# Optimization experiments

Hardware: AMD Instinct MI355X
Metric: run time of the kernel (lower is better)

The kernel has to match this reference:

```python
import jax, jax.numpy as jnp
import numpy as np

B, C_IN, N_IN, N_OUT = 4, 64, 8192, 8192
D1, F, H = 4, 15, 16384  # d+1, filter_size, max_hash_cnt
C_MID, C_OUT = 64, 64
LEAK = 0.01


def setup_inputs() -> dict:
    key = jax.random.key(0)
    ks = jax.random.split(key, 10)
    features = jax.random.normal(ks[0], (B, C_IN, N_IN), jnp.float32)
    in_barycentric = jax.random.uniform(ks[1], (B, D1, N_IN), dtype=jnp.float32)
    # global flat lattice offsets: local vertex id in [0,H) plus per-batch base b*(H+1)
    local_off = jax.random.randint(ks[2], (B, D1, N_IN), 0, H)
    base = (jnp.arange(B, dtype=jnp.int64) * (H + 1))[:, None, None]
    in_lattice_offset = local_off.astype(jnp.int64) + base
    # neighbor ids in [-1, H); -1 means missing -> maps to zero padding slot after +1
    blur_neighbors = (jax.random.randint(ks[3], (B, F, H), 0, H + 1) - 1).astype(jnp.int64)
    out_barycentric = jax.random.uniform(ks[4], (B, D1, N_OUT), dtype=jnp.float32)
    out_lattice_offset = jax.random.randint(ks[5], (B, D1, N_OUT), 0, H).astype(jnp.int64)
    # blur conv params: layer0 Conv2d(C_IN,C_MID,(F,1)) + LeakyReLU, layer1 Conv2d(C_MID,C_OUT,(1,1)) no relu
    W0 = jax.random.normal(ks[6], (C_MID, C_IN, F), jnp.float32) * 0.05
    b0 = jax.random.normal(ks[7], (C_MID,), jnp.float32) * 0.01
    W1 = jax.random.normal(ks[8], (C_OUT, C_MID), jnp.float32) * 0.1
    b1 = jax.random.normal(ks[9], (C_OUT,), jnp.float32) * 0.01
    bias = jnp.zeros((C_OUT,), jnp.float32)  # slice bias, initialized to zeros as in module
    return dict(features=features, in_barycentric=in_barycentric,
                in_lattice_offset=in_lattice_offset, blur_neighbors=blur_neighbors,
                out_barycentric=out_barycentric, out_lattice_offset=out_lattice_offset,
                W0=W0, b0=b0, W1=W1, b1=b1, bias=bias)


def reference(features, in_barycentric, in_lattice_offset, blur_neighbors,
              out_barycentric, out_lattice_offset, W0, b0, W1, b1, bias):
    b_sz, c_in, n_in = features.shape
    max_hash = blur_neighbors.shape[-1]
    # ---- splat: scatter-sum barycentric-weighted features onto lattice vertices ----
    vals = in_barycentric[:, None, :, :] * features[:, :, None, :]      # (B,C,d1,N)
    vals = vals.transpose(0, 2, 3, 1).reshape(-1, c_in)                  # (B*d1*N, C)
    idx = (in_lattice_offset + 1).reshape(-1)                            # (B*d1*N,)
    splat = jax.ops.segment_sum(vals, idx, num_segments=b_sz * (max_hash + 1))
    splat = splat.reshape(b_sz, max_hash + 1, c_in).transpose(0, 2, 1)   # (B,C,H+1)
    # normalization: splat of all-ones feature
    one_splat = jax.ops.segment_sum(in_barycentric.reshape(-1), idx,
                                    num_segments=b_sz * (max_hash + 1))
    one_splat = one_splat.reshape(b_sz, max_hash + 1)
    splat = splat / (one_splat + 1e-5)[:, None, :]
    # ---- blur: gather F neighbors per vertex, then conv over the filter axis ----
    spread = jax.vmap(lambda s, n: s[:, n])(splat, blur_neighbors + 1)   # (B,C,F,H)
    h0 = jnp.einsum('bcfh,ocf->boh', spread, W0) + b0[None, :, None]     # (B,C_mid,H)
    h0 = jnp.where(h0 > 0, h0, LEAK * h0)                                # LeakyReLU
    feat_blurred = jnp.einsum('boh,po->bph', h0, W1) + b1[None, :, None] # (B,C_out,H)
    # ---- slice: barycentric-weighted gather back to output points ----
    tmp = jax.vmap(lambda f, o: f[:, o])(feat_blurred, out_lattice_offset)  # (B,C_out,d1,N_out)
    sliced = (out_barycentric[:, None, :, :] * tmp).sum(axis=2)
    sliced = sliced + bias[None, :, None]
    return sliced
```

## Files before the change

kernel.cpp:

```cpp
#include <hip/hip_runtime.h>

#define NB 4
#define C_IN 64
#define N_IN 8192
#define N_OUT 8192
#define D1 4
#define FS 15
#define HSZ 16384
#define C_MID 64
#define C_OUT 64
#define LEAK 0.01f
#define CAP 24

#define NVERT (NB*(HSZ+1))

typedef __attribute__((ext_vector_type(8))) short short8;
typedef __attribute__((ext_vector_type(4))) float floatx4;

#define SPLATB_OFF 0
#define SPLATB_FL  (NVERT*32)
#define W0B_OFF    (SPLATB_OFF + SPLATB_FL)
#define W0B_FL     (C_MID*C_IN*FS/2)
#define W1B_OFF    (W0B_OFF + W0B_FL)
#define W1B_FL     (C_OUT*C_MID/2)
#define BREG_OFF   (W1B_OFF + W1B_FL)
#define FEATB_OFF  (BREG_OFF)
#define FEATB_FL   (NB*N_IN*32)
#define CNT_OFF    (FEATB_OFF + FEATB_FL)
#define CNT_FL     (NVERT)
#define ENTID_OFF  (CNT_OFF + CNT_FL)
#define ENT_FL     (NVERT*CAP)
#define ENTW_OFF   (ENTID_OFF + ENT_FL)
#define FB_OFF     (BREG_OFF)
#define FB_FL      (NB*HSZ*32)

__device__ inline ushort f2bf(float x) {
    uint u = __float_as_uint(x);
    return (ushort)((u + 0x7FFF + ((u >> 16) & 1)) >> 16);
}
__device__ inline float bf2f(ushort b) {
    return __uint_as_float(((uint)b) << 16);
}

__global__ __launch_bounds__(256) void prep(const float* __restrict__ feat,
                                            const float* __restrict__ W0,
                                            const float* __restrict__ W1,
                                            const int* __restrict__ off,
                                            const float* __restrict__ bary,
                                            ushort* __restrict__ featB,
                                            ushort* __restrict__ W0b,
                                            ushort* __restrict__ W1b,
                                            int* __restrict__ cnt,
                                            int* __restrict__ ent_id,
                                            float* __restrict__ ent_w) {
    __shared__ float t[64 * 65];
    const int blk = blockIdx.x;
    const int tid = threadIdx.x;
    if (blk < 512) {
        const int b  = blk >> 7;
        const int nb = (blk & 127) << 6;
        const int l  = tid & 63;
        const int g  = tid >> 6;
#pragma unroll
        for (int i = 0; i < 16; ++i) {
            int c = g * 16 + i;
            t[c * 65 + l] = feat[((size_t)(b * 64 + c)) * N_IN + nb + l];
        }
        __syncthreads();
#pragma unroll
        for (int i = 0; i < 16; ++i) {
            int n = g * 16 + i;
            featB[((size_t)(b * N_IN) + nb + n) * 64 + l] = f2bf(t[l * 65 + n]);
        }
    } else if (blk < 1024) {
        int e = (blk - 512) * 256 + tid;
        int v = off[e] + 1;
        int n = e % N_IN;
        int b = e / (D1 * N_IN);
        int slot = atomicAdd(&cnt[v], 1);
        if (slot < CAP) {
            ent_id[v * CAP + slot] = b * N_IN + n;
            ent_w [v * CAP + slot] = bary[e];
        }
    } else {
        int e = (blk - 1024) * 256 + tid;
        if (e < C_MID * C_IN * FS) {
            int f = e >> 12;
            int o = (e >> 6) & 63;
            int c = e & 63;
            W0b[e] = f2bf(W0[(o * 64 + c) * FS + f]);
        } else {
            int e2 = e - C_MID * C_IN * FS;
            W1b[e2] = f2bf(W1[e2]);
        }
    }
}

__global__ __launch_bounds__(256) void gather_splat(const ushort* __restrict__ featB,
                                                    const int* __restrict__ cnt,
                                                    const int* __restrict__ ent_id,
                                                    const float* __restrict__ ent_w,
                                                    ushort* __restrict__ splatB) {
    const int v    = blockIdx.x * 4 + (threadIdx.x >> 6);
    const int lane = threadIdx.x & 63;
    int c = cnt[v];
    if (c > CAP) c = CAP;
    float acc = 0.f, sw = 0.f;
    for (int e = 0; e < c; ++e) {
        int   pt = ent_id[v * CAP + e];
        float wt = ent_w [v * CAP + e];
        acc += wt * bf2f(featB[(size_t)pt * 64 + lane]);
        sw  += wt;
    }
    splatB[(size_t)v * 64 + lane] = f2bf(acc / (sw + 1e-5f));
}

#define LSTR 80
__global__ __launch_bounds__(256, 4) void blur_mfma(const ushort* __restrict__ splatB,
                                                    const int* __restrict__ nbr,
                                                    const ushort* __restrict__ W0b,
                                                    const ushort* __restrict__ W1b,
                                                    const float* __restrict__ b0,
                                                    const float* __restrict__ b1,
                                                    ushort* __restrict__ fb) {
    __shared__ ushort As[2][64 * LSTR];
    __shared__ ushort Xs[2][64 * LSTR];

    const int tid = threadIdx.x;
    const int p   = blockIdx.x;
    const int b   = p & 3;
    const int hb  = (p >> 2) << 6;

    const int lane = tid & 63;
    const int w    = tid >> 6;
    const int m    = lane & 15;
    const int q    = lane >> 4;

    const int r0   = tid >> 3;
    const int r1   = r0 + 32;
    const int sseg = (tid & 7) * 8;

    const int* nbase = nbr + (b * FS) * HSZ + hb;
    const size_t sbase = (size_t)b * (HSZ + 1) * 64;

    {
        int v0 = nbase[r0] + 1, v1 = nbase[r1] + 1;
        *(short8*)&As[0][r0 * LSTR + sseg] = *(const short8*)&W0b[r0 * 64 + sseg];
        *(short8*)&As[0][r1 * LSTR + sseg] = *(const short8*)&W0b[r1 * 64 + sseg];
        *(short8*)&Xs[0][r0 * LSTR + sseg] = *(const short8*)&splatB[sbase + (size_t)v0 * 64 + sseg];
        *(short8*)&Xs[0][r1 * LSTR + sseg] = *(const short8*)&splatB[sbase + (size_t)v1 * 64 + sseg];
    }
    int nv0 = nbase[HSZ + r0] + 1;
    int nv1 = nbase[HSZ + r1] + 1;
    __syncthreads();

    floatx4 acc[4] = {};

#pragma unroll
    for (int f = 0; f < FS; ++f) {
        const int cur = f & 1, nxt = cur ^ 1;
        short8 pa0, pa1, px0, px1;
        int nn0 = 0, nn1 = 0;
        if (f < FS - 1) {
            const ushort* w0n = W0b + (f + 1) * 4096;
            pa0 = *(const short8*)&w0n[r0 * 64 + sseg];
            pa1 = *(const short8*)&w0n[r1 * 64 + sseg];
            px0 = *(const short8*)&splatB[sbase + (size_t)nv0 * 64 + sseg];
            px1 = *(const short8*)&splatB[sbase + (size_t)nv1 * 64 + sseg];
            if (f < FS - 2) {
                nn0 = nbase[(f + 2) * HSZ + r0] + 1;
                nn1 = nbase[(f + 2) * HSZ + r1] + 1;
            }
        }
#pragma unroll
        for (int ch = 0; ch < 2; ++ch) {
            const int ko = ch * 32 + q * 8;
            short8 a = *(const short8*)&As[cur][(w * 16 + m) * LSTR + ko];
#pragma unroll
            for (int t = 0; t < 4; ++t) {
                short8 bb = *(const short8*)&Xs[cur][(t * 16 + m) * LSTR + ko];
                acc[t] = __builtin_amdgcn_mfma_f32_16x16x32_bf16(a, bb, acc[t], 0, 0, 0);
            }
        }
        if (f < FS - 1) {
            *(short8*)&As[nxt][r0 * LSTR + sseg] = pa0;
            *(short8*)&As[nxt][r1 * LSTR + sseg] = pa1;
            *(short8*)&Xs[nxt][r0 * LSTR + sseg] = px0;
            *(short8*)&Xs[nxt][r1 * LSTR + sseg] = px1;
            nv0 = nn0; nv1 = nn1;
        }
        __syncthreads();
    }

    *(short8*)&As[0][r0 * LSTR + sseg] = *(const short8*)&W1b[r0 * 64 + sseg];
    *(short8*)&As[0][r1 * LSTR + sseg] = *(const short8*)&W1b[r1 * 64 + sseg];
    {
        const float4 b0v = *(const float4*)(b0 + w * 16 + q * 4);
#pragma unroll
        for (int t = 0; t < 4; ++t) {
            float v0 = acc[t][0] + b0v.x; v0 = v0 > 0.f ? v0 : LEAK * v0;
            float v1 = acc[t][1] + b0v.y; v1 = v1 > 0.f ? v1 : LEAK * v1;
            float v2 = acc[t][2] + b0v.z; v2 = v2 > 0.f ? v2 : LEAK * v2;
            float v3 = acc[t][3] + b0v.w; v3 = v3 > 0.f ? v3 : LEAK * v3;
            ushort4 hv;
            hv.x = f2bf(v0); hv.y = f2bf(v1); hv.z = f2bf(v2); hv.w = f2bf(v3);
            *(ushort4*)&Xs[0][(t * 16 + m) * LSTR + w * 16 + q * 4] = hv;
        }
    }
    __syncthreads();

    floatx4 acc2[4] = {};
#pragma unroll
    for (int ch = 0; ch < 2; ++ch) {
        const int ko = ch * 32 + q * 8;
        short8 a2 = *(const short8*)&As[0][(w * 16 + m) * LSTR + ko];
#pragma unroll
        for (int t = 0; t < 4; ++t) {
            short8 b2 = *(const short8*)&Xs[0][(t * 16 + m) * LSTR + ko];
            acc2[t] = __builtin_amdgcn_mfma_f32_16x16x32_bf16(a2, b2, acc2[t], 0, 0, 0);
        }
    }

    {
        const float4 b1v = *(const float4*)(b1 + w * 16 + q * 4);
#pragma unroll
        for (int t = 0; t < 4; ++t) {
            ushort4 ov;
            ov.x = f2bf(acc2[t][0] + b1v.x);
            ov.y = f2bf(acc2[t][1] + b1v.y);
            ov.z = f2bf(acc2[t][2] + b1v.z);
            ov.w = f2bf(acc2[t][3] + b1v.w);
            *(ushort4*)&Xs[1][(t * 16 + m) * LSTR + w * 16 + q * 4] = ov;
        }
    }
    __syncthreads();
    *(short8*)&fb[((size_t)(b * HSZ) + hb + r0) * 64 + sseg] = *(const short8*)&Xs[1][r0 * LSTR + sseg];
    *(short8*)&fb[((size_t)(b * HSZ) + hb + r1) * 64 + sseg] = *(const short8*)&Xs[1][r1 * LSTR + sseg];
}

__global__ __launch_bounds__(256) void slice_kernel(const ushort* __restrict__ fb,
                                                    const float* __restrict__ ob,
                                                    const int* __restrict__ off,
                                                    const float* __restrict__ bias,
                                                    float* __restrict__ out) {
    __shared__ float tile[64 * 65];
    const int blk  = blockIdx.x;
    const int b    = blk & 3;
    const int nb   = (blk >> 2) << 6;
    const int lane = threadIdx.x & 63;
    const int w    = threadIdx.x >> 6;

    const float bs = bias[lane];
#pragma unroll 4
    for (int t = 0; t < 16; ++t) {
        int nl = w * 16 + t;
        int n  = nb + nl;
        float acc = bs;
#pragma unroll
        for (int j = 0; j < D1; ++j) {
            float wj = ob[(b * D1 + j) * N_OUT + n];
            int   oj = off[(b * D1 + j) * N_OUT + n];
            acc += wj * bf2f(fb[((size_t)b * HSZ + oj) * 64 + lane]);
        }
        tile[lane * 65 + nl] = acc;
    }
    __syncthreads();
#pragma unroll
    for (int r = 0; r < 16; ++r) {
        int p = w * 16 + r;
        out[((size_t)(b * 64 + p)) * N_OUT + nb + lane] = tile[p * 65 + lane];
    }
}

extern "C" void kernel_launch(void* const* d_in, const int* in_sizes, int n_in,
                              void* d_out, int out_size, void* d_ws, size_t ws_size,
                              hipStream_t stream) {
    const float* features = (const float*)d_in[0];
    const float* in_bary  = (const float*)d_in[1];
    const int*   in_off   = (const int*)d_in[2];
    const int*   nbr      = (const int*)d_in[3];
    const float* out_bary = (const float*)d_in[4];
    const int*   out_off  = (const int*)d_in[5];
    const float* W0       = (const float*)d_in[6];
    const float* b0       = (const float*)d_in[7];
    const float* W1       = (const float*)d_in[8];
    const float* b1       = (const float*)d_in[9];
    const float* bias     = (const float*)d_in[10];

    float*  ws     = (float*)d_ws;
    ushort* splatB = (ushort*)(ws + SPLATB_OFF);
    ushort* W0b    = (ushort*)(ws + W0B_OFF);
    ushort* W1b    = (ushort*)(ws + W1B_OFF);
    ushort* featB  = (ushort*)(ws + FEATB_OFF);
    int*    cnt    = (int*)(ws + CNT_OFF);
    int*    ent_id = (int*)(ws + ENTID_OFF);
    float*  ent_w  = ws + ENTW_OFF;
    ushort* fb     = (ushort*)(ws + FB_OFF);

    hipMemsetAsync(cnt, 0, (size_t)CNT_FL * sizeof(int), stream);

    prep<<<1280, 256, 0, stream>>>(features, W0, W1, in_off, in_bary,
                                   featB, W0b, W1b, cnt, ent_id, ent_w);
    gather_splat<<<NVERT / 4, 256, 0, stream>>>(featB, cnt, ent_id, ent_w, splatB);
    blur_mfma<<<NB * (HSZ / 64), 256, 0, stream>>>(splatB, nbr, W0b, W1b, b0, b1, fb);
    slice_kernel<<<NB * (N_OUT / 64), 256, 0, stream>>>(fb, out_bary, out_off, bias, (float*)d_out);
}
```

Measured before the change: 140.5 us.

## Pre-swizzle blur weights into MFMA fragment layout and widen tile to 128 vertices

The prep kernel now writes W0 and W1 in bf16, pre-arranged into per-lane MFMA A-fragment order. The blur kernel can then load weights straight into registers and no longer stages them through shared memory. Each block now handles 128 lattice vertices instead of 64, with each wave computing a 32x64 output tile. This halves the block count and reuses each B fragment across two MFMAs. Results are written directly to global memory rather than through an LDS staging pass, at the cost of more registers (launch bounds lowered to 2) and less coalesced output stores.

Measured after the change: 141.1 us. About the same (+0.4%).

```diff
diff --git a/kernel.cpp b/kernel.cpp
--- a/kernel.cpp
+++ b/kernel.cpp
@@ -19,11 +19,11 @@
 
 #define SPLATB_OFF 0
 #define SPLATB_FL  (NVERT*32)
-#define W0B_OFF    (SPLATB_OFF + SPLATB_FL)
-#define W0B_FL     (C_MID*C_IN*FS/2)
-#define W1B_OFF    (W0B_OFF + W0B_FL)
-#define W1B_FL     (C_OUT*C_MID/2)
-#define BREG_OFF   (W1B_OFF + W1B_FL)
+#define W0F_OFF    (SPLATB_OFF + SPLATB_FL)
+#define W0F_FL     (C_MID*C_IN*FS/2)
+#define W1F_OFF    (W0F_OFF + W0F_FL)
+#define W1F_FL     (C_OUT*C_MID/2)
+#define BREG_OFF   (W1F_OFF + W1F_FL)
 #define FEATB_OFF  (BREG_OFF)
 #define FEATB_FL   (NB*N_IN*32)
 #define CNT_OFF    (FEATB_OFF + FEATB_FL)
@@ -48,8 +48,8 @@
                                             const int* __restrict__ off,
                                             const float* __restrict__ bary,
                                             ushort* __restrict__ featB,
-                                            ushort* __restrict__ W0b,
-                                            ushort* __restrict__ W1b,
+                                            ushort* __restrict__ W0f,
+                                            ushort* __restrict__ W1f,
                                             int* __restrict__ cnt,
                                             int* __restrict__ ent_id,
                                             float* __restrict__ ent_w) {
@@ -85,13 +85,23 @@
     } else {
         int e = (blk - 1024) * 256 + tid;
         if (e < C_MID * C_IN * FS) {
-            int f = e >> 12;
-            int o = (e >> 6) & 63;
-            int c = e & 63;
-            W0b[e] = f2bf(W0[(o * 64 + c) * FS + f]);
+            int j    = e & 7;
+            int lane = (e >> 3) & 63;
+            int ch   = (e >> 9) & 1;
+            int ot   = (e >> 10) & 3;
+            int f    = e >> 12;
+            int o = ot * 16 + (lane & 15);
+            int c = ch * 32 + ((lane >> 4) & 3) * 8 + j;
+            W0f[e] = f2bf(W0[(o * 64 + c) * FS + f]);
         } else {
-            int e2 = e - C_MID * C_IN * FS;
-            W1b[e2] = f2bf(W1[e2]);
+            int e2   = e - C_MID * C_IN * FS;
+            int j    = e2 & 7;
+            int lane = (e2 >> 3) & 63;
+            int ch   = (e2 >> 9) & 1;
+            int pt   = (e2 >> 10) & 3;
+            int p = pt * 16 + (lane & 15);
+            int o = ch * 32 + ((lane >> 4) & 3) * 8 + j;
+            W1f[e2] = f2bf(W1[p * 64 + o]);
         }
     }
 }
@@ -115,127 +125,143 @@
     splatB[(size_t)v * 64 + lane] = f2bf(acc / (sw + 1e-5f));
 }
 
-#define LSTR 80
-__global__ __launch_bounds__(256, 4) void blur_mfma(const ushort* __restrict__ splatB,
+#define XSTR 72
+__global__ __launch_bounds__(256, 2) void blur_mfma(const ushort* __restrict__ splatB,
                                                     const int* __restrict__ nbr,
-                                                    const ushort* __restrict__ W0b,
-                                                    const ushort* __restrict__ W1b,
+                                                    const ushort* __restrict__ W0f,
+                                                    const ushort* __restrict__ W1f,
                                                     const float* __restrict__ b0,
                                                     const float* __restrict__ b1,
                                                     ushort* __restrict__ fb) {
-    __shared__ ushort As[2][64 * LSTR];
-    __shared__ ushort Xs[2][64 * LSTR];
+    __shared__ ushort Xs[2][128 * XSTR];
 
     const int tid = threadIdx.x;
     const int p   = blockIdx.x;
     const int b   = p & 3;
-    const int hb  = (p >> 2) << 6;
+    const int hb  = (p >> 2) << 7;
 
     const int lane = tid & 63;
     const int w    = tid >> 6;
+    const int ow   = w & 1;
+    const int hw   = w >> 1;
     const int m    = lane & 15;
     const int q    = lane >> 4;
 
-    const int r0   = tid >> 3;
-    const int r1   = r0 + 32;
-    const int sseg = (tid & 7) * 8;
+    const int r    = tid >> 1;
+    const int sseg = (tid & 1) * 32;
 
     const int* nbase = nbr + (b * FS) * HSZ + hb;
     const size_t sbase = (size_t)b * (HSZ + 1) * 64;
 
+    short8 acur[2][2], anxt[2][2];
+#pragma unroll
+    for (int ot = 0; ot < 2; ++ot)
+#pragma unroll
+        for (int ch = 0; ch < 2; ++ch)
+            acur[ot][ch] = *(const short8*)&W0f[(((ow * 2 + ot) * 2 + ch) * 64 + lane) * 8];
+
     {
-        int v0 = nbase[r0] + 1, v1 = nbase[r1] + 1;
-        *(short8*)&As[0][r0 * LSTR + sseg] = *(const short8*)&W0b[r0 * 64 + sseg];
-        *(short8*)&As[0][r1 * LSTR + sseg] = *(const short8*)&W0b[r1 * 64 + sseg];
-        *(short8*)&Xs[0][r0 * LSTR + sseg] = *(const short8*)&splatB[sbase + (size_t)v0 * 64 + sseg];
-        *(short8*)&Xs[0][r1 * LSTR + sseg] = *(const short8*)&splatB[sbase + (size_t)v1 * 64 + sseg];
-    }
-    int nv0 = nbase[HSZ + r0] + 1;
-    int nv1 = nbase[HSZ + r1] + 1;
+        int v = nbase[r] + 1;
+        const ushort* row = splatB + sbase + (size_t)v * 64 + sseg;
+#pragma unroll
+        for (int k = 0; k < 4; ++k)
+            *(short8*)&Xs[0][r * XSTR + sseg + k * 8] = *(const short8*)&row[k * 8];
+    }
+    int nv = nbase[HSZ + r] + 1;
     __syncthreads();
 
-    floatx4 acc[4] = {};
-
-#pragma unroll
+    floatx4 acc[2][4] = {};
+
     for (int f = 0; f < FS; ++f) {
         const int cur = f & 1, nxt = cur ^ 1;
-        short8 pa0, pa1, px0, px1;
-        int nn0 = 0, nn1 = 0;
+        short8 px[4];
+        int nn = 0;
         if (f < FS - 1) {
-            const ushort* w0n = W0b + (f + 1) * 4096;
-            pa0 = *(const short8*)&w0n[r0 * 64 + sseg];
-            pa1 = *(const short8*)&w0n[r1 * 64 + sseg];
-            px0 = *(const short8*)&splatB[sbase + (size_t)nv0 * 64 + sseg];
-            px1 = *(const short8*)&splatB[sbase + (size_t)nv1 * 64 + sseg];
-            if (f < FS - 2) {
-                nn0 = nbase[(f + 2) * HSZ + r0] + 1;
-                nn1 = nbase[(f + 2) * HSZ + r1] + 1;
-            }
+            const ushort* row = splatB + sbase + (size_t)nv * 64 + sseg;
+#pragma unroll
+            for (int k = 0; k < 4; ++k) px[k] = *(const short8*)&row[k * 8];
+#pragma unroll
+            for (int ot = 0; ot < 2; ++ot)
+#pragma unroll
+                for (int ch = 0; ch < 2; ++ch)
+                    anxt[ot][ch] = *(const short8*)
+                        &W0f[((((f + 1) * 4 + ow * 2 + ot) * 2 + ch) * 64 + lane) * 8];
+            if (f < FS - 2) nn = nbase[(f + 2) * HSZ + r] + 1;
         }
 #pragma unroll
         for (int ch = 0; ch < 2; ++ch) {
             const int ko = ch * 32 + q * 8;
-            short8 a = *(const short8*)&As[cur][(w * 16 + m) * LSTR + ko];
-#pragma unroll
-            for (int t = 0; t < 4; ++t) {
-                short8 bb = *(const short8*)&Xs[cur][(t * 16 + m) * LSTR + ko];
-                acc[t] = __builtin_amdgcn_mfma_f32_16x16x32_bf16(a, bb, acc[t], 0, 0, 0);
+#pragma unroll
+            for (int ht = 0; ht < 4; ++ht) {
+                short8 bb = *(const short8*)&Xs[cur][(hw * 64 + ht * 16 + m) * XSTR + ko];
+                acc[0][ht] = __builtin_amdgcn_mfma_f32_16x16x32_bf16(acur[0][ch], bb, acc[0][ht], 0, 0, 0);
+                acc[1][ht] = __builtin_amdgcn_mfma_f32_16x16x32_bf16(acur[1][ch], bb, acc[1][ht], 0, 0, 0);
             }
         }
         if (f < FS - 1) {
-            *(short8*)&As[nxt][r0 * LSTR + sseg] = pa0;
-            *(short8*)&As[nxt][r1 * LSTR + sseg] = pa1;
-            *(short8*)&Xs[nxt][r0 * LSTR + sseg] = px0;
-            *(short8*)&Xs[nxt][r1 * LSTR + sseg] = px1;
-            nv0 = nn0; nv1 = nn1;
+#pragma unroll
+            for (int k = 0; k < 4; ++k)
+                *(short8*)&Xs[nxt][r * XSTR + sseg + k * 8] = px[k];
+            nv = nn;
+#pragma unroll
+            for (int ot = 0; ot < 2; ++ot)
+#pragma unroll
+                for (int ch = 0; ch < 2; ++ch)
+                    acur[ot][ch] = anxt[ot][ch];
         }
         __syncthreads();
     }
 
-    *(short8*)&As[0][r0 * LSTR + sseg] = *(const short8*)&W1b[r0 * 64 + sseg];
-    *(short8*)&As[0][r1 * LSTR + sseg] = *(const short8*)&W1b[r1 * 64 + sseg];
-    {
-        const float4 b0v = *(const float4*)(b0 + w * 16 + q * 4);
-#pragma unroll
-        for (int t = 0; t < 4; ++t) {
-            float v0 = acc[t][0] + b0v.x; v0 = v0 > 0.f ? v0 : LEAK * v0;
-            float v1 = acc[t][1] + b0v.y; v1 = v1 > 0.f ? v1 : LEAK * v1;
-            float v2 = acc[t][2] + b0v.z; v2 = v2 > 0.f ? v2 : LEAK * v2;
-            float v3 = acc[t][3] + b0v.w; v3 = v3 > 0.f ? v3 : LEAK * v3;
+    short8 a2[2][2];
+#pragma unroll
+    for (int pt = 0; pt < 2; ++pt)
+#pragma unroll
+        for (int ch = 0; ch < 2; ++ch)
+            a2[pt][ch] = *(const short8*)&W1f[(((ow * 2 + pt) * 2 + ch) * 64 + lane) * 8];
+
+    ushort* Hs = &Xs[0][0];
+#pragma unroll
+    for (int ot = 0; ot < 2; ++ot) {
+        const float4 b0v = *(const float4*)(b0 + ow * 32 + ot * 16 + q * 4);
+#pragma unroll
+        for (int ht = 0; ht < 4; ++ht) {
+            float v0 = acc[ot][ht][0] + b0v.x; v0 = v0 > 0.f ? v0 : LEAK * v0;
+            float v1 = acc[ot][ht][1] + b0v.y; v1 = v1 > 0.f ? v1 : LEAK * v1;
+            float v2 = acc[ot][ht][2] + b0v.z; v2 = v2 > 0.f ? v2 : LEAK * v2;
+            float v3 = acc[ot][ht][3] + b0v.w; v3 = v3 > 0.f ? v3 : LEAK * v3;
             ushort4 hv;
             hv.x = f2bf(v0); hv.y = f2bf(v1); hv.z = f2bf(v2); hv.w = f2bf(v3);
-            *(ushort4*)&Xs[0][(t * 16 + m) * LSTR + w * 16 + q * 4] = hv;
+            *(ushort4*)&Hs[(hw * 64 + ht * 16 + m) * XSTR + ow * 32 + ot * 16 + q * 4] = hv;
         }
     }
     __syncthreads();
 
-    floatx4 acc2[4] = {};
+    floatx4 acc2[2][4] = {};
 #pragma unroll
     for (int ch = 0; ch < 2; ++ch) {
         const int ko = ch * 32 + q * 8;
-        short8 a2 = *(const short8*)&As[0][(w * 16 + m) * LSTR + ko];
-#pragma unroll
-        for (int t = 0; t < 4; ++t) {
-            short8 b2 = *(const short8*)&Xs[0][(t * 16 + m) * LSTR + ko];
-            acc2[t] = __builtin_amdgcn_mfma_f32_16x16x32_bf16(a2, b2, acc2[t], 0, 0, 0);
-        }
-    }
-
-    {
-        const float4 b1v = *(const float4*)(b1 + w * 16 + q * 4);
-#pragma unroll
-        for (int t = 0; t < 4; ++t) {
+#pragma unroll
+        for (int ht = 0; ht < 4; ++ht) {
+            short8 b2 = *(const short8*)&Hs[(hw * 64 + ht * 16 + m) * XSTR + ko];
+            acc2[0][ht] = __builtin_amdgcn_mfma_f32_16x16x32_bf16(a2[0][ch], b2, acc2[0][ht], 0, 0, 0);
+            acc2[1][ht] = __builtin_amdgcn_mfma_f32_16x16x32_bf16(a2[1][ch], b2, acc2[1][ht], 0, 0, 0);
+        }
+    }
+
+#pragma unroll
+    for (int pt = 0; pt < 2; ++pt) {
+        const float4 b1v = *(const float4*)(b1 + ow * 32 + pt * 16 + q * 4);
+#pragma unroll
+        for (int ht = 0; ht < 4; ++ht) {
             ushort4 ov;
-            ov.x = f2bf(acc2[t][0] + b1v.x);
-            ov.y = f2bf(acc2[t][1] + b1v.y);
-            ov.z = f2bf(acc2[t][2] + b1v.z);
-            ov.w = f2bf(acc2[t][3] + b1v.w);
-            *(ushort4*)&Xs[1][(t * 16 + m) * LSTR + w * 16 + q * 4] = ov;
-        }
-    }
-    __syncthreads();
-    *(short8*)&fb[((size_t)(b * HSZ) + hb + r0) * 64 + sseg] = *(const short8*)&Xs[1][r0 * LSTR + sseg];
-    *(short8*)&fb[((size_t)(b * HSZ) + hb + r1) * 64 + sseg] = *(const short8*)&Xs[1][r1 * LSTR + sseg];
+            ov.x = f2bf(acc2[pt][ht][0] + b1v.x);
+            ov.y = f2bf(acc2[pt][ht][1] + b1v.y);
+            ov.z = f2bf(acc2[pt][ht][2] + b1v.z);
+            ov.w = f2bf(acc2[pt][ht][3] + b1v.w);
+            *(ushort4*)&fb[((size_t)(b * HSZ) + hb + hw * 64 + ht * 16 + m) * 64
+                           + ow * 32 + pt * 16 + q * 4] = ov;
+        }
+    }
 }
 
 __global__ __launch_bounds__(256) void slice_kernel(const ushort* __restrict__ fb,
@@ -289,8 +315,8 @@
 
     float*  ws     = (float*)d_ws;
     ushort* splatB = (ushort*)(ws + SPLATB_OFF);
-    ushort* W0b    = (ushort*)(ws + W0B_OFF);
-    ushort* W1b    = (ushort*)(ws + W1B_OFF);
+    ushort* W0f    = (ushort*)(ws + W0F_OFF);
+    ushort* W1f    = (ushort*)(ws + W1F_OFF);
     ushort* featB  = (ushort*)(ws + FEATB_OFF);
     int*    cnt    = (int*)(ws + CNT_OFF);
     int*    ent_id = (int*)(ws + ENTID_OFF);
@@ -300,8 +326,8 @@
     hipMemsetAsync(cnt, 0, (size_t)CNT_FL * sizeof(int), stream);
 
     prep<<<1280, 256, 0, stream>>>(features, W0, W1, in_off, in_bary,
-                                   featB, W0b, W1b, cnt, ent_id, ent_w);
+                                   featB, W0f, W1f, cnt, ent_id, ent_w);
     gather_splat<<<NVERT / 4, 256, 0, stream>>>(featB, cnt, ent_id, ent_w, splatB);
-    blur_mfma<<<NB * (HSZ / 64), 256, 0, stream>>>(splatB, nbr, W0b, W1b, b0, b1, fb);
+    blur_mfma<<<NB * (HSZ / 128), 256, 0, stream>>>(splatB, nbr, W0f, W1f, b0, b1, fb);
     slice_kernel<<<NB * (N_OUT / 64), 256, 0, stream>>>(fb, out_bary, out_off, bias, (float*)d_out);
 }
```
